# Kernel tuning notes

Hardware: AMD Instinct MI355X
Metric: run time of the kernel (lower is better)

The kernel has to match this reference:

```python
import jax, jax.numpy as jnp
import numpy as np

N_SEQ = 500
SEQ_LEN = 200
TOTAL = N_SEQ * SEQ_LEN   # 100000 rows in M
NCOL = 1024               # alignment columns
DCOL = 512                # column feature dim
NOUT = 26                 # len(ALPHABET) + 1


def setup_inputs() -> dict:
    key = jax.random.key(0)
    k1, k2, k3 = jax.random.split(key, 3)
    M = jax.random.normal(k1, (TOTAL, NCOL), dtype=jnp.float32)
    columns = jax.random.normal(k2, (NCOL, DCOL), dtype=jnp.float32)
    sequence_lengths = jnp.full((N_SEQ,), SEQ_LEN, dtype=jnp.int64)
    W = jax.random.normal(k3, (DCOL, NOUT), dtype=jnp.float32) * 0.05
    b = jnp.zeros((NOUT,), dtype=jnp.float32)
    return {"M": M, "columns": columns, "sequence_lengths": sequence_lengths, "W": W, "b": b}


def reference(M, columns, sequence_lengths, W, b):
    total, ncol = M.shape
    nseq = sequence_lengths.shape[0]
    ncol_f = jnp.asarray(ncol, dtype=M.dtype)

    # soft-argmax: expected column index per residue, [total, 1]
    colrange = jnp.arange(ncol, dtype=M.dtype)[:, None]
    soft_argmax = M @ colrange

    # gaps between consecutive residues, [total-1, 1]
    gaps = soft_argmax[1:] - soft_argmax[:-1] - 1.0

    # sequence boundary positions: cumsum(lengths)[:-1] - 1 mark last residue of
    # each sequence except the final one; drop those gap entries.
    cs = jnp.cumsum(sequence_lengths)                      # [nseq]
    removed = cs[:-1] - 1                                   # [nseq-1]
    mask = jnp.ones((total - 1,), dtype=bool).at[removed].set(False)
    n_keep = total - 1 - (nseq - 1)                          # static
    keep_idx = jnp.nonzero(mask, size=n_keep)[0]
    gaps_in = gaps[keep_idx] / ncol_f                        # [n_keep, 1]

    # gap before first residue of each sequence: rows [0, cs[0], ..., cs[-2]]
    start_idx = jnp.concatenate([jnp.zeros((1,), dtype=cs.dtype), cs[:-1]])
    gaps_start = soft_argmax[start_idx] / ncol_f             # [nseq, 1]

    # gap after last residue of each sequence: rows cs-1
    gaps_end = (ncol_f - soft_argmax[cs - 1] - 1.0) / ncol_f  # [nseq, 1]

    relative_positions = soft_argmax / ncol_f                # [total, 1]

    # col_decoder: Dense(26, softmax)
    col_dist = jax.nn.softmax(columns @ W + b, axis=-1)      # [ncol, 26]

    return (relative_positions, gaps_start, gaps_in, gaps_end, col_dist)
```

## Files before the change

### kernel.cpp

```cpp
#include <hip/hip_runtime.h>
#include <hip/hip_bf16.h>


__global__ void __launch_bounds__(256) soft_argmax_kernel(
    const float* __restrict__ M, float* __restrict__ sa,
    float* __restrict__ relpos, int total, int ncol, float inv_ncol) {
  int wave = (blockIdx.x * blockDim.x + threadIdx.x) >> 6;
  int lane = threadIdx.x & 63;
  if (wave >= total) return;

  const float4* rowv = reinterpret_cast<const float4*>(M + (size_t)wave * ncol);
  int nchunk = ncol >> 2;
  float acc = 0.0f;
  for (int c = lane; c < nchunk; c += 64) {
    float4 u = rowv[c];
    float j = (float)(c << 2);
    acc = fmaf(u.x, j + 0.0f, acc);
    acc = fmaf(u.y, j + 1.0f, acc);
    acc = fmaf(u.z, j + 2.0f, acc);
    acc = fmaf(u.w, j + 3.0f, acc);
  }
  #pragma unroll
  for (int off = 32; off > 0; off >>= 1) acc += __shfl_xor(acc, off, 64);
  if (lane == 0) {
    sa[wave] = acc;
    relpos[wave] = acc * inv_ncol;
  }
}

__global__ void scan_kernel(const int* __restrict__ len32, int* __restrict__ cs,
                            int nseq) {
  __shared__ int buf[1024];
  __shared__ int hi_nonzero;
  int t = threadIdx.x;
  if (t == 0) hi_nonzero = 0;
  __syncthreads();
  if (t < (nseq >> 1)) {
    if (len32[2 * t + 1] != 0) atomicOr(&hi_nonzero, 1);
  }
  __syncthreads();
  bool is64 = (hi_nonzero == 0);
  buf[t] = (t < nseq) ? (is64 ? len32[2 * t] : len32[t]) : 0;
  __syncthreads();
  for (int off = 1; off < nseq; off <<= 1) {
    int add = (t >= off) ? buf[t - off] : 0;
    __syncthreads();
    buf[t] += add;
    __syncthreads();
  }
  if (t < nseq) cs[t] = buf[t];
}

__global__ void gaps_kernel(const float* __restrict__ sa,
                            const int* __restrict__ cs,
                            float* __restrict__ gstart,
                            float* __restrict__ gin,
                            float* __restrict__ gend,
                            float inv_ncol, float ncolf) {
  int s = blockIdx.x;
  int end = cs[s];
  int prev = (s == 0) ? 0 : cs[s - 1];
  if (threadIdx.x == 0) {
    gstart[s] = sa[prev] * inv_ncol;
    gend[s]   = (ncolf - sa[end - 1] - 1.0f) * inv_ncol;
  }
  int ngap = end - 1 - prev;
  int outbase = prev - s;
  for (int t = threadIdx.x; t < ngap; t += blockDim.x) {
    gin[outbase + t] = (sa[prev + t + 1] - sa[prev + t] - 1.0f) * inv_ncol;
  }
}

__global__ void __launch_bounds__(256) coldist_kernel(
    const float* __restrict__ columns, const float* __restrict__ W,
    const float* __restrict__ b, float* __restrict__ out, int dcol, int nout) {
  const int ROWS = 8;
  extern __shared__ float rowsf[];

  int t = threadIdx.x;
  int row0 = blockIdx.x * ROWS;
  const float4* Cv = reinterpret_cast<const float4*>(columns + (size_t)row0 * dcol);
  float4* Lv = reinterpret_cast<float4*>(rowsf);
  int nCv = (ROWS * dcol) >> 2;
  for (int i = t; i < nCv; i += 256) Lv[i] = Cv[i];
  float* bf = rowsf + ROWS * dcol;
  if (t < 32) bf[t] = (t < nout) ? b[t] : 0.0f;
  __syncthreads();

  int o = t & 31;
  int rl = t >> 5;
  int oc = (o < nout) ? o : (nout - 1);
  const float* rp = rowsf + rl * dcol;
  float acc = bf[oc];
  #pragma unroll 4
  for (int k = 0; k < dcol; k++) acc = fmaf(rp[k], W[k * nout + oc], acc);
  if (o >= nout) acc = -3.0e38f;

  float mx = acc;
  #pragma unroll
  for (int off = 16; off > 0; off >>= 1) mx = fmaxf(mx, __shfl_xor(mx, off, 32));
  float e = (o < nout) ? __expf(acc - mx) : 0.0f;
  float ssum = e;
  #pragma unroll
  for (int off = 16; off > 0; off >>= 1) ssum += __shfl_xor(ssum, off, 32);
  if (o < nout)
    out[(size_t)(row0 + rl) * nout + o] = e / ssum;
}

extern "C" void kernel_launch(void* const* d_in, const int* in_sizes, int n_in,
                              void* d_out, int out_size, void* d_ws,
                              size_t ws_size, hipStream_t stream) {
  const float* M       = (const float*)d_in[0];
  const float* columns = (const float*)d_in[1];
  const int*   seqlen  = (const int*)d_in[2];
  const float* W       = (const float*)d_in[3];
  const float* b       = (const float*)d_in[4];

  int nout  = in_sizes[4];
  int dcol  = in_sizes[3] / nout;
  int ncol  = in_sizes[1] / dcol;
  int total = in_sizes[0] / ncol;
  int nseq  = in_sizes[2];

  float* out     = (float*)d_out;
  float* out_rel = out;
  float* out_gs  = out_rel + total;
  float* out_gi  = out_gs + nseq;
  float* out_ge  = out_gi + (total - nseq);
  float* out_cd  = out_ge + nseq;

  float* sa = (float*)d_ws;
  int* cs = (int*)((char*)d_ws + (((size_t)total * 4 + 255) & ~(size_t)255));

  float inv_ncol = 1.0f / (float)ncol;

  int blocksA = (total + 3) / 4;
  hipLaunchKernelGGL(soft_argmax_kernel, dim3(blocksA), dim3(256), 0, stream,
                     M, sa, out_rel, total, ncol, inv_ncol);
  hipLaunchKernelGGL(scan_kernel, dim3(1), dim3(1024), 0, stream, seqlen, cs,
                     nseq);
  hipLaunchKernelGGL(gaps_kernel, dim3(nseq), dim3(256), 0, stream, sa, cs,
                     out_gs, out_gi, out_ge, inv_ncol, (float)ncol);
  const int ROWS = 8;
  size_t lds = (size_t)ROWS * dcol * 4 + 32 * 4;
  hipLaunchKernelGGL(coldist_kernel, dim3(ncol / ROWS), dim3(256), lds, stream,
                     columns, W, b, out_cd, dcol, nout);
}
```

Before: 582.4 us.

## Fuse column decoder into persistent soft-argmax kernel and drop scan launch

Merges the column-softmax decoder and the soft-argmax row reduction into one launch, with dedicated leading blocks for the decoder and a grid-stride persistent loop over M rows. Each row's four float4 loads are issued together to raise memory-level parallelism. The separate scan kernel is removed; each gaps block computes its own prefix sum and reads the scaled relpos directly, avoiding the workspace array. This cuts launch count and serialization, but gaps are now derived from pre-scaled values, which may differ slightly in rounding.

```diff
diff --git a/kernel.cpp b/kernel.cpp
--- a/kernel.cpp
+++ b/kernel.cpp
@@ -2,109 +2,141 @@
 #include <hip/hip_bf16.h>
 
 
-__global__ void __launch_bounds__(256) soft_argmax_kernel(
-    const float* __restrict__ M, float* __restrict__ sa,
-    float* __restrict__ relpos, int total, int ncol, float inv_ncol) {
-  int wave = (blockIdx.x * blockDim.x + threadIdx.x) >> 6;
-  int lane = threadIdx.x & 63;
-  if (wave >= total) return;
+#define CD_ROWS 8
+#define CD_MAXD 512
+#define A_BLOCKS 1920
 
-  const float4* rowv = reinterpret_cast<const float4*>(M + (size_t)wave * ncol);
+__global__ void __launch_bounds__(256) fused_main_kernel(
+    const float* __restrict__ M, const float* __restrict__ columns,
+    const float* __restrict__ W, const float* __restrict__ b,
+    float* __restrict__ relpos, float* __restrict__ out_cd, int total,
+    int ncol, float inv_ncol, int dcol, int nout, int nblk_cd) {
+  __shared__ float smem_f[CD_ROWS * CD_MAXD + 64];
+  int t = threadIdx.x;
+
+  if ((int)blockIdx.x < nblk_cd) {
+    int row0 = blockIdx.x * CD_ROWS;
+    bool lds_ok = (dcol <= CD_MAXD);
+    if (lds_ok) {
+      const float4* Cv =
+          reinterpret_cast<const float4*>(columns + (size_t)row0 * dcol);
+      float4* Lv = reinterpret_cast<float4*>(smem_f);
+      int nCv = (CD_ROWS * dcol) >> 2;
+      for (int i = t; i < nCv; i += 256) Lv[i] = Cv[i];
+    }
+    float* bf = smem_f + CD_ROWS * CD_MAXD;
+    if (t < 32) bf[t] = (t < nout) ? b[t] : 0.0f;
+    __syncthreads();
+
+    int o = t & 31;
+    int rl = t >> 5;
+    int oc = (o < nout) ? o : (nout - 1);
+    const float* rp = lds_ok ? (smem_f + rl * dcol)
+                             : (columns + (size_t)(row0 + rl) * dcol);
+    float acc = bf[oc];
+    #pragma unroll 4
+    for (int k = 0; k < dcol; k++) acc = fmaf(rp[k], W[k * nout + oc], acc);
+    if (o >= nout) acc = -3.0e38f;
+
+    float mx = acc;
+    #pragma unroll
+    for (int off = 16; off > 0; off >>= 1)
+      mx = fmaxf(mx, __shfl_xor(mx, off, 32));
+    float e = (o < nout) ? __expf(acc - mx) : 0.0f;
+    float ssum = e;
+    #pragma unroll
+    for (int off = 16; off > 0; off >>= 1) ssum += __shfl_xor(ssum, off, 32);
+    if (o < nout) out_cd[(size_t)(row0 + rl) * nout + o] = e / ssum;
+    return;
+  }
+
+  int lane = t & 63;
+  int wavesPerBlk = blockDim.x >> 6;
+  int wslot = (blockIdx.x - nblk_cd) * wavesPerBlk + (t >> 6);
+  int nwaves = (gridDim.x - nblk_cd) * wavesPerBlk;
   int nchunk = ncol >> 2;
-  float acc = 0.0f;
-  for (int c = lane; c < nchunk; c += 64) {
-    float4 u = rowv[c];
-    float j = (float)(c << 2);
-    acc = fmaf(u.x, j + 0.0f, acc);
-    acc = fmaf(u.y, j + 1.0f, acc);
-    acc = fmaf(u.z, j + 2.0f, acc);
-    acc = fmaf(u.w, j + 3.0f, acc);
-  }
-  #pragma unroll
-  for (int off = 32; off > 0; off >>= 1) acc += __shfl_xor(acc, off, 64);
-  if (lane == 0) {
-    sa[wave] = acc;
-    relpos[wave] = acc * inv_ncol;
+
+  for (int row = wslot; row < total; row += nwaves) {
+    const float4* rowv =
+        reinterpret_cast<const float4*>(M + (size_t)row * ncol);
+    float acc = 0.0f;
+    if (nchunk == 256) {
+      float4 u0 = rowv[lane];
+      float4 u1 = rowv[lane + 64];
+      float4 u2 = rowv[lane + 128];
+      float4 u3 = rowv[lane + 192];
+      float j0 = (float)(lane << 2);
+      float j1 = j0 + 256.0f, j2 = j0 + 512.0f, j3 = j0 + 768.0f;
+      acc = fmaf(u0.x, j0, acc);
+      acc = fmaf(u0.y, j0 + 1.0f, acc);
+      acc = fmaf(u0.z, j0 + 2.0f, acc);
+      acc = fmaf(u0.w, j0 + 3.0f, acc);
+      acc = fmaf(u1.x, j1, acc);
+      acc = fmaf(u1.y, j1 + 1.0f, acc);
+      acc = fmaf(u1.z, j1 + 2.0f, acc);
+      acc = fmaf(u1.w, j1 + 3.0f, acc);
+      acc = fmaf(u2.x, j2, acc);
+      acc = fmaf(u2.y, j2 + 1.0f, acc);
+      acc = fmaf(u2.z, j2 + 2.0f, acc);
+      acc = fmaf(u2.w, j2 + 3.0f, acc);
+      acc = fmaf(u3.x, j3, acc);
+      acc = fmaf(u3.y, j3 + 1.0f, acc);
+      acc = fmaf(u3.z, j3 + 2.0f, acc);
+      acc = fmaf(u3.w, j3 + 3.0f, acc);
+    } else {
+      for (int c = lane; c < nchunk; c += 64) {
+        float4 u = rowv[c];
+        float j = (float)(c << 2);
+        acc = fmaf(u.x, j + 0.0f, acc);
+        acc = fmaf(u.y, j + 1.0f, acc);
+        acc = fmaf(u.z, j + 2.0f, acc);
+        acc = fmaf(u.w, j + 3.0f, acc);
+      }
+    }
+    #pragma unroll
+    for (int off = 32; off > 0; off >>= 1) acc += __shfl_xor(acc, off, 64);
+    if (lane == 0) relpos[row] = acc * inv_ncol;
   }
 }
 
-__global__ void scan_kernel(const int* __restrict__ len32, int* __restrict__ cs,
-                            int nseq) {
-  __shared__ int buf[1024];
-  __shared__ int hi_nonzero;
+__global__ void __launch_bounds__(256) gaps_kernel(
+    const float* __restrict__ relpos, const int* __restrict__ len32,
+    float* __restrict__ gstart, float* __restrict__ gin,
+    float* __restrict__ gend, int nseq, float inv_ncol) {
+  __shared__ int sh_red[4];
+  __shared__ int sh_prev, sh_len, sh_hi;
+  int s = blockIdx.x;
   int t = threadIdx.x;
-  if (t == 0) hi_nonzero = 0;
+
+  if (t == 0) sh_hi = 0;
   __syncthreads();
-  if (t < (nseq >> 1)) {
-    if (len32[2 * t + 1] != 0) atomicOr(&hi_nonzero, 1);
+  if (t < (nseq >> 1) && len32[2 * t + 1] != 0) atomicOr(&sh_hi, 1);
+  __syncthreads();
+  bool is64 = (sh_hi == 0);
+
+  int part = 0;
+  for (int k = t; k < nseq; k += 256) {
+    int L = is64 ? len32[2 * k] : len32[k];
+    if (k < s) part += L;
+    if (k == s) sh_len = L;
   }
+  #pragma unroll
+  for (int off = 32; off > 0; off >>= 1) part += __shfl_xor(part, off, 64);
+  if ((t & 63) == 0) sh_red[t >> 6] = part;
   __syncthreads();
-  bool is64 = (hi_nonzero == 0);
-  buf[t] = (t < nseq) ? (is64 ? len32[2 * t] : len32[t]) : 0;
-  __syncthreads();
-  for (int off = 1; off < nseq; off <<= 1) {
-    int add = (t >= off) ? buf[t - off] : 0;
-    __syncthreads();
-    buf[t] += add;
-    __syncthreads();
-  }
-  if (t < nseq) cs[t] = buf[t];
-}
-
-__global__ void gaps_kernel(const float* __restrict__ sa,
-                            const int* __restrict__ cs,
-                            float* __restrict__ gstart,
-                            float* __restrict__ gin,
-                            float* __restrict__ gend,
-                            float inv_ncol, float ncolf) {
-  int s = blockIdx.x;
-  int end = cs[s];
-  int prev = (s == 0) ? 0 : cs[s - 1];
-  if (threadIdx.x == 0) {
-    gstart[s] = sa[prev] * inv_ncol;
-    gend[s]   = (ncolf - sa[end - 1] - 1.0f) * inv_ncol;
-  }
-  int ngap = end - 1 - prev;
-  int outbase = prev - s;
-  for (int t = threadIdx.x; t < ngap; t += blockDim.x) {
-    gin[outbase + t] = (sa[prev + t + 1] - sa[prev + t] - 1.0f) * inv_ncol;
-  }
-}
-
-__global__ void __launch_bounds__(256) coldist_kernel(
-    const float* __restrict__ columns, const float* __restrict__ W,
-    const float* __restrict__ b, float* __restrict__ out, int dcol, int nout) {
-  const int ROWS = 8;
-  extern __shared__ float rowsf[];
-
-  int t = threadIdx.x;
-  int row0 = blockIdx.x * ROWS;
-  const float4* Cv = reinterpret_cast<const float4*>(columns + (size_t)row0 * dcol);
-  float4* Lv = reinterpret_cast<float4*>(rowsf);
-  int nCv = (ROWS * dcol) >> 2;
-  for (int i = t; i < nCv; i += 256) Lv[i] = Cv[i];
-  float* bf = rowsf + ROWS * dcol;
-  if (t < 32) bf[t] = (t < nout) ? b[t] : 0.0f;
+  if (t == 0) sh_prev = sh_red[0] + sh_red[1] + sh_red[2] + sh_red[3];
   __syncthreads();
 
-  int o = t & 31;
-  int rl = t >> 5;
-  int oc = (o < nout) ? o : (nout - 1);
-  const float* rp = rowsf + rl * dcol;
-  float acc = bf[oc];
-  #pragma unroll 4
-  for (int k = 0; k < dcol; k++) acc = fmaf(rp[k], W[k * nout + oc], acc);
-  if (o >= nout) acc = -3.0e38f;
-
-  float mx = acc;
-  #pragma unroll
-  for (int off = 16; off > 0; off >>= 1) mx = fmaxf(mx, __shfl_xor(mx, off, 32));
-  float e = (o < nout) ? __expf(acc - mx) : 0.0f;
-  float ssum = e;
-  #pragma unroll
-  for (int off = 16; off > 0; off >>= 1) ssum += __shfl_xor(ssum, off, 32);
-  if (o < nout)
-    out[(size_t)(row0 + rl) * nout + o] = e / ssum;
+  int prev = sh_prev;
+  int L = sh_len;
+  int end = prev + L;
+  if (t == 0) {
+    gstart[s] = relpos[prev];
+    gend[s] = 1.0f - inv_ncol - relpos[end - 1];
+  }
+  int outbase = prev - s;
+  for (int g = t; g < L - 1; g += 256)
+    gin[outbase + g] = relpos[prev + g + 1] - relpos[prev + g] - inv_ncol;
 }
 
 extern "C" void kernel_launch(void* const* d_in, const int* in_sizes, int n_in,
@@ -129,20 +161,12 @@
   float* out_ge  = out_gi + (total - nseq);
   float* out_cd  = out_ge + nseq;
 
-  float* sa = (float*)d_ws;
-  int* cs = (int*)((char*)d_ws + (((size_t)total * 4 + 255) & ~(size_t)255));
+  float inv_ncol = 1.0f / (float)ncol;
+  int nblk_cd = (ncol + CD_ROWS - 1) / CD_ROWS;
 
-  float inv_ncol = 1.0f / (float)ncol;
-
-  int blocksA = (total + 3) / 4;
-  hipLaunchKernelGGL(soft_argmax_kernel, dim3(blocksA), dim3(256), 0, stream,
-                     M, sa, out_rel, total, ncol, inv_ncol);
-  hipLaunchKernelGGL(scan_kernel, dim3(1), dim3(1024), 0, stream, seqlen, cs,
-                     nseq);
-  hipLaunchKernelGGL(gaps_kernel, dim3(nseq), dim3(256), 0, stream, sa, cs,
-                     out_gs, out_gi, out_ge, inv_ncol, (float)ncol);
-  const int ROWS = 8;
-  size_t lds = (size_t)ROWS * dcol * 4 + 32 * 4;
-  hipLaunchKernelGGL(coldist_kernel, dim3(ncol / ROWS), dim3(256), lds, stream,
-                     columns, W, b, out_cd, dcol, nout);
+  hipLaunchKernelGGL(fused_main_kernel, dim3(nblk_cd + A_BLOCKS), dim3(256), 0,
+                     stream, M, columns, W, b, out_rel, out_cd, total, ncol,
+                     inv_ncol, dcol, nout, nblk_cd);
+  hipLaunchKernelGGL(gaps_kernel, dim3(nseq), dim3(256), 0, stream, out_rel,
+                     seqlen, out_gs, out_gi, out_ge, nseq, inv_ncol);
 }
```

After: 555.5 us. 4.6% less time.
